# Optimization experiments

Measured on AMD Instinct MI355X. Metric: run time of the kernel, lower is better.

## Reference

```python
import jax, jax.numpy as jnp
import numpy as np

D = 1024
H = 16
HD = D // H
S = 2048
B = 2
INNER = 4 * D
EPS = 1e-5


def _layernorm(x, w, b):
    mu = jnp.mean(x, axis=-1, keepdims=True)
    var = jnp.mean(jnp.square(x - mu), axis=-1, keepdims=True)
    return (x - mu) * jax.lax.rsqrt(var + EPS) * w + b


def _rope(x, cos, sin):
    # x: [B, S, H, HD]; cos/sin: [S, HD//2]
    xe, xo = x[..., 0::2], x[..., 1::2]
    c = cos[None, :, None, :]
    s = sin[None, :, None, :]
    oe = xe * c - xo * s
    oo = xe * s + xo * c
    return jnp.stack([oe, oo], axis=-1).reshape(x.shape)


def setup_inputs() -> dict:
    key = jax.random.key(0)
    ks = jax.random.split(key, 12)
    hidden_states = jax.random.normal(ks[0], (B, S, D), dtype=jnp.float32)
    time_step_emb = jax.random.normal(ks[1], (B, 6 * D), dtype=jnp.float32)
    # causal additive mask [1,1,S,S]
    causal = jnp.tril(jnp.ones((S, S), dtype=bool))
    attention_mask = jnp.where(causal, 0.0, -1e9).astype(jnp.float32)[None, None]
    # proper RoPE tables
    inv_freq = 1.0 / (10000.0 ** (np.arange(0, HD, 2, dtype=np.float32) / HD))
    t = np.arange(S, dtype=np.float32)
    freqs = np.outer(t, inv_freq)  # [S, HD//2]
    rope_cos = jnp.asarray(np.cos(freqs))
    rope_sin = jnp.asarray(np.sin(freqs))
    p = 0.02
    params = dict(
        ln1_w=jnp.ones((D,), jnp.float32), ln1_b=jnp.zeros((D,), jnp.float32),
        ln2_w=jnp.ones((D,), jnp.float32), ln2_b=jnp.zeros((D,), jnp.float32),
        c_attn_w=jax.random.normal(ks[2], (D, 3 * D), jnp.float32) * p,
        c_attn_b=jnp.zeros((3 * D,), jnp.float32),
        c_proj_w=jax.random.normal(ks[3], (D, D), jnp.float32) * p,
        c_proj_b=jnp.zeros((D,), jnp.float32),
        fc_w=jax.random.normal(ks[4], (D, INNER), jnp.float32) * p,
        fc_b=jnp.zeros((INNER,), jnp.float32),
        proj_w=jax.random.normal(ks[5], (INNER, D), jnp.float32) * p,
        proj_b=jnp.zeros((D,), jnp.float32),
        scale_shift_table=jax.random.normal(ks[6], (6, D), jnp.float32) / np.sqrt(D),
    )
    return dict(hidden_states=hidden_states, attention_mask=attention_mask,
                time_step_emb=time_step_emb, rope_cos=rope_cos, rope_sin=rope_sin,
                **params)


def reference(hidden_states, attention_mask, time_step_emb, rope_cos, rope_sin,
              ln1_w, ln1_b, ln2_w, ln2_b, c_attn_w, c_attn_b, c_proj_w, c_proj_b,
              fc_w, fc_b, proj_w, proj_b, scale_shift_table):
    b = hidden_states.shape[0]
    mods = scale_shift_table[None] + time_step_emb.reshape(b, 6, D)  # [B,6,D]
    sh_msa, sc_msa, g_msa, sh_mlp, sc_mlp, g_mlp = [mods[:, i:i + 1] for i in range(6)]

    residual = hidden_states
    h = _layernorm(hidden_states, ln1_w, ln1_b) * (1.0 + sc_msa) + sh_msa

    qkv = h @ c_attn_w + c_attn_b  # [B,S,3D]
    q, k, v = jnp.split(qkv, 3, axis=-1)
    q = _rope(q.reshape(b, S, H, HD), rope_cos, rope_sin)
    k = _rope(k.reshape(b, S, H, HD), rope_cos, rope_sin)
    v = v.reshape(b, S, H, HD)
    scores = jnp.einsum('bqhd,bkhd->bhqk', q, k) / np.sqrt(float(HD))
    scores = scores + attention_mask
    attn = jax.nn.softmax(scores, axis=-1)
    out = jnp.einsum('bhqk,bkhd->bqhd', attn, v).reshape(b, S, D)
    attn_out = out @ c_proj_w + c_proj_b

    hidden = attn_out * g_msa + residual
    residual = hidden
    h = _layernorm(hidden, ln2_w, ln2_b) * (1.0 + sc_mlp) + sh_mlp
    h = jax.nn.gelu(h @ fc_w + fc_b, approximate=True)  # gelu_new (tanh approx)
    h = h @ proj_w + proj_b
    return h * g_mlp + residual
```

## Files before the change

### kernel.cpp

```cpp
#include <hip/hip_runtime.h>
#include <hip/hip_bf16.h>

#define D_MODEL 1024
#define N_HEADS 16
#define HEAD_DIM 64
#define SEQ 2048
#define BATCH 2
#define INNER_DIM 4096
#define ROWS (BATCH*SEQ)

using f32x4  = __attribute__((ext_vector_type(4))) float;
using bf16x8 = __attribute__((ext_vector_type(8))) short;

__device__ __forceinline__ void gl_lds16(const void* g, void* l) {
  __builtin_amdgcn_global_load_lds(
      (const __attribute__((address_space(1))) void*)g,
      (__attribute__((address_space(3))) void*)l, 16, 0, 0);
}

__device__ __forceinline__ float bf2f(unsigned short u) {
  union { unsigned int i; float f; } v; v.i = ((unsigned int)u) << 16; return v.f;
}
__device__ __forceinline__ unsigned short f2bf(float f) {
  union { float f; unsigned int i; } v; v.f = f;
  unsigned int x = v.i;
  return (unsigned short)((x + 0x7fffu + ((x >> 16) & 1u)) >> 16);
}

__device__ __forceinline__ float exp2fast(float x) {
  return __builtin_amdgcn_exp2f(x);
}

__device__ __forceinline__ float gelu_tanh(float x) {
  float x3 = x * x * x;
  float z = 0.7978845608028654f * (x + 0.044715f * x3);
  z = fminf(z, 15.0f);
  float e = __expf(2.0f * z);
  float th = (e - 1.0f) / (e + 1.0f);
  return 0.5f * x * (1.0f + th);
}

__global__ void transpose_convert(const float* __restrict__ in,
                                  unsigned short* __restrict__ out,
                                  int K, int N) {
  __shared__ float tile[32][33];
  int n0 = blockIdx.x * 32, k0 = blockIdx.y * 32;
  int tx = threadIdx.x, ty = threadIdx.y;
#pragma unroll
  for (int i = 0; i < 4; i++)
    tile[ty + i * 8][tx] = in[(size_t)(k0 + ty + i * 8) * N + n0 + tx];
  __syncthreads();
#pragma unroll
  for (int i = 0; i < 4; i++)
    out[(size_t)(n0 + ty + i * 8) * K + k0 + tx] = f2bf(tile[tx][ty + i * 8]);
}

template<int SH_IDX, int SC_IDX>
__global__ void ln_mod_kernel(const float* __restrict__ x,
                              const float* __restrict__ lw,
                              const float* __restrict__ lb,
                              const float* __restrict__ sst,
                              const float* __restrict__ temb,
                              unsigned short* __restrict__ out) {
  int row = blockIdx.x;
  int b = row >> 11;
  int t = threadIdx.x;
  const float* xr = x + (size_t)row * D_MODEL;
  float4 v = ((const float4*)xr)[t];
  float s = v.x + v.y + v.z + v.w;
  float s2 = v.x * v.x + v.y * v.y + v.z * v.z + v.w * v.w;
#pragma unroll
  for (int o = 1; o < 64; o <<= 1) { s += __shfl_xor(s, o); s2 += __shfl_xor(s2, o); }
  __shared__ float red[8];
  int wid = t >> 6, lane = t & 63;
  if (lane == 0) { red[wid] = s; red[4 + wid] = s2; }
  __syncthreads();
  s = red[0] + red[1] + red[2] + red[3];
  s2 = red[4] + red[5] + red[6] + red[7];
  float mu = s * (1.0f / D_MODEL);
  float var = s2 * (1.0f / D_MODEL) - mu * mu;
  float rs = rsqrtf(var + 1e-5f);
  int d0 = t * 4;
  float xv[4] = { v.x, v.y, v.z, v.w };
  ushort4 ov;
  unsigned short* po = (unsigned short*)&ov;
#pragma unroll
  for (int j = 0; j < 4; j++) {
    int d = d0 + j;
    float ln = (xv[j] - mu) * rs * lw[d] + lb[d];
    float sc = sst[SC_IDX * D_MODEL + d] + temb[b * 6 * D_MODEL + SC_IDX * D_MODEL + d];
    float sh = sst[SH_IDX * D_MODEL + d] + temb[b * 6 * D_MODEL + SH_IDX * D_MODEL + d];
    po[j] = f2bf(ln * (1.0f + sc) + sh);
  }
  *((ushort4*)(out + (size_t)row * D_MODEL + d0)) = ov;
}

enum { EPI_QKV = 0, EPI_RES = 1, EPI_GELU = 2, EPI_FINAL = 3 };

template<int EPI, int BMF>
__global__ __launch_bounds__(256, 2)
void gemm_kernel(const unsigned short* __restrict__ A,
                 const unsigned short* __restrict__ Bt,
                 const float* __restrict__ bias,
                 void* __restrict__ Cout,
                 int N, int K,
                 const float* __restrict__ sst,
                 const float* __restrict__ temb,
                 int g_idx,
                 const float* __restrict__ res,
                 const float* __restrict__ cosb,
                 const float* __restrict__ sinb) {
  constexpr int NBUF = 4;
  __shared__ unsigned short Alds[NBUF][BMF * 32 * 32];
  __shared__ unsigned short Blds[NBUF][128 * 32];
  const int t = threadIdx.x;
  const int w = t >> 6, l = t & 63;
  const int lg = l >> 4, ll = l & 15;
  const int wm = w >> 1, wn = w & 1;

  const int nx = gridDim.x;
  const int nwg = nx * gridDim.y;
  const int lid = blockIdx.y * nx + blockIdx.x;
  const int nid = (lid & 7) * (nwg >> 3) + (lid >> 3);
  const int m0 = (nid / nx) * (BMF * 32), n0 = (nid % nx) * 128;

  f32x4 acc[BMF][4] = {};

  auto stage = [&](int k0, int buf) {
#pragma unroll
    for (int i = 0; i < BMF / 2; i++) {
      int c = i * 256 + t;
      int row = c >> 2, ch = c & 3;
      int chs = ch ^ ((row >> 1) & 3);
      gl_lds16(A + (size_t)(m0 + row) * K + k0 + chs * 8, (char*)&Alds[buf][0] + c * 16);
    }
#pragma unroll
    for (int i = 0; i < 2; i++) {
      int c = i * 256 + t;
      int row = c >> 2, ch = c & 3;
      int chs = ch ^ ((row >> 1) & 3);
      gl_lds16(Bt + (size_t)(n0 + row) * K + k0 + chs * 8, (char*)&Blds[buf][0] + c * 16);
    }
  };

  auto comp = [&](int buf) {
    asm volatile("" ::: "memory");
    bf16x8 af[BMF], bfr[4];
#pragma unroll
    for (int mf = 0; mf < BMF; mf++) {
      int row = wm * (BMF * 16) + mf * 16 + ll;
      int ch = lg ^ ((row >> 1) & 3);
      af[mf] = *(const bf16x8*)((const char*)&Alds[buf][0] + row * 64 + ch * 16);
    }
#pragma unroll
    for (int nf = 0; nf < 4; nf++) {
      int row = wn * 64 + nf * 16 + ll;
      int ch = lg ^ ((row >> 1) & 3);
      bfr[nf] = *(const bf16x8*)((const char*)&Blds[buf][0] + row * 64 + ch * 16);
    }
#pragma unroll
    for (int mf = 0; mf < BMF; mf++)
#pragma unroll
      for (int nf = 0; nf < 4; nf++)
        acc[mf][nf] = __builtin_amdgcn_mfma_f32_16x16x32_bf16(af[mf], bfr[nf], acc[mf][nf], 0, 0, 0);
    asm volatile("" ::: "memory");
  };

  const int nk = K >> 5;
  stage(0, 0); stage(32, 1); stage(64, 2);
  int it = 0;
  for (; it + 3 < nk; ++it) {
    stage((it + 3) * 32, (it + 3) & 3);
    if constexpr (BMF == 4) asm volatile("s_waitcnt vmcnt(12)" ::: "memory");
    else                    asm volatile("s_waitcnt vmcnt(9)" ::: "memory");
    __builtin_amdgcn_s_barrier();
    comp(it & 3);
    __builtin_amdgcn_s_barrier();
  }
  if constexpr (BMF == 4) asm volatile("s_waitcnt vmcnt(8)" ::: "memory");
  else                    asm volatile("s_waitcnt vmcnt(6)" ::: "memory");
  __builtin_amdgcn_s_barrier(); comp(it & 3); __builtin_amdgcn_s_barrier(); ++it;
  if constexpr (BMF == 4) asm volatile("s_waitcnt vmcnt(4)" ::: "memory");
  else                    asm volatile("s_waitcnt vmcnt(3)" ::: "memory");
  __builtin_amdgcn_s_barrier(); comp(it & 3); __builtin_amdgcn_s_barrier(); ++it;
  asm volatile("s_waitcnt vmcnt(0)" ::: "memory");
  __builtin_amdgcn_s_barrier(); comp(it & 3); __builtin_amdgcn_s_barrier();

#pragma unroll
  for (int mf = 0; mf < BMF; mf++) {
#pragma unroll
    for (int nf = 0; nf < 4; nf++) {
      int col = n0 + wn * 64 + nf * 16 + ll;
      float bv = bias[col];
#pragma unroll
      for (int r = 0; r < 4; r++) {
        int row = m0 + wm * (BMF * 16) + mf * 16 + lg * 4 + r;
        float v = acc[mf][nf][r] + bv;
        if constexpr (EPI == EPI_QKV) {
          if (col < 2048) {
            float vp = __shfl_xor(v, 1);
            int sp = row & (SEQ - 1);
            int ip = (col & 63) >> 1;
            float cz = cosb[sp * 32 + ip], sz = sinb[sp * 32 + ip];
            float ov = (col & 1) ? (vp * sz + v * cz) : (v * cz - vp * sz);
            if (col < 1024) ov *= 0.18033688011112042f;
            v = ov;
          }
          ((unsigned short*)Cout)[(size_t)row * N + col] = f2bf(v);
        } else if constexpr (EPI == EPI_GELU) {
          ((unsigned short*)Cout)[(size_t)row * N + col] = f2bf(gelu_tanh(v));
        } else {
          int bb = row >> 11;
          float g = sst[g_idx * D_MODEL + col] + temb[bb * 6 * D_MODEL + g_idx * D_MODEL + col];
          ((float*)Cout)[(size_t)row * N + col] = v * g + res[(size_t)row * N + col];
        }
      }
    }
  }
}

__global__ __launch_bounds__(256, 4)
void attn_kernel(const unsigned short* __restrict__ qkv,
                 unsigned short* __restrict__ attn_o) {
  __shared__ unsigned short Klds[2][64 * 64];
  __shared__ unsigned short Vt[2][64 * 64];
  __shared__ unsigned short Plds[4][16 * 64];

  const int id = blockIdx.x;
  const int bh = id & 31;
  const int b = bh >> 4, h = bh & 15;
  const int q0 = (id >> 5) * 64;
  const int t = threadIdx.x;
  const int w = t >> 6, l = t & 63;
  const int lg = l >> 4, ll = l & 15;
  const int qw0 = q0 + w * 16;
  const int q_lane = qw0 + ll;

  bf16x8 qf[2];
  {
    const unsigned short* qb = qkv + (size_t)(b * SEQ + q_lane) * 3072 + h * 64;
    qf[0] = *(const bf16x8*)(qb + lg * 8);
    qf[1] = *(const bf16x8*)(qb + 32 + lg * 8);
  }

  const int kp = t & 31, dg = t >> 5;

  f32x4 oacc[4] = {};
  float mrun = -1e30f, lrun = 0.0f;

  {
#pragma unroll
    for (int i = 0; i < 2; i++) {
      int c = i * 256 + t;
      int kr = c >> 3, cc = c & 7;
      gl_lds16(qkv + (size_t)(b * SEQ + kr) * 3072 + 1024 + h * 64 + (cc ^ (kr & 7)) * 8,
               (char*)&Klds[0][0] + c * 16);
    }
    const unsigned short* vp = qkv + (size_t)(b * SEQ + 2 * kp) * 3072 + 2048 + h * 64 + dg * 8;
    union { uint4 u; unsigned short s[8]; } a0, a1;
    a0.u = *(const uint4*)vp;
    a1.u = *(const uint4*)(vp + 3072);
    unsigned int* vt32 = (unsigned int*)&Vt[0][0];
#pragma unroll
    for (int i = 0; i < 8; i++)
      vt32[(dg * 8 + i) * 32 + (((kp >> 2) ^ i) << 2) + (kp & 3)] =
          (unsigned int)a0.s[i] | ((unsigned int)a1.s[i] << 16);
  }
  __syncthreads();

  int buf = 0;
  for (int k0 = 0; k0 <= q0; k0 += 64) {
    const bool has_next = (k0 + 64 <= q0);
    union { uint4 u; unsigned short s[8]; } n0, n1;
    if (has_next) {
#pragma unroll
      for (int i = 0; i < 2; i++) {
        int c = i * 256 + t;
        int kr = c >> 3, cc = c & 7;
        gl_lds16(qkv + (size_t)(b * SEQ + k0 + 64 + kr) * 3072 + 1024 + h * 64 + (cc ^ (kr & 7)) * 8,
                 (char*)&Klds[buf ^ 1][0] + c * 16);
      }
      const unsigned short* vp =
          qkv + (size_t)(b * SEQ + k0 + 64 + 2 * kp) * 3072 + 2048 + h * 64 + dg * 8;
      n0.u = *(const uint4*)vp;
      n1.u = *(const uint4*)(vp + 3072);
    }

    f32x4 s[4] = {};
#pragma unroll
    for (int kk = 0; kk < 2; kk++) {
#pragma unroll
      for (int nf = 0; nf < 4; nf++) {
        int key = nf * 16 + ll;
        int cc = (kk * 4 + lg) ^ (key & 7);
        bf16x8 kf = *(const bf16x8*)((const char*)&Klds[buf][0] + key * 128 + cc * 16);
        s[nf] = __builtin_amdgcn_mfma_f32_16x16x32_bf16(kf, qf[kk], s[nf], 0, 0, 0);
      }
    }
    if (k0 == q0) {
#pragma unroll
      for (int nf = 0; nf < 4; nf++) {
        int key = k0 + nf * 16 + lg * 4;
#pragma unroll
        for (int r = 0; r < 4; r++)
          if (key + r > q_lane) s[nf][r] = -1e30f;
      }
    }
    float mx = -1e30f;
#pragma unroll
    for (int nf = 0; nf < 4; nf++)
#pragma unroll
      for (int r = 0; r < 4; r++) mx = fmaxf(mx, s[nf][r]);
    mx = fmaxf(mx, __shfl_xor(mx, 16));
    mx = fmaxf(mx, __shfl_xor(mx, 32));
    float mnew = fmaxf(mrun, mx);
    float alpha = exp2fast(mrun - mnew);
    mrun = mnew;
    float ps = 0.0f;
#pragma unroll
    for (int nf = 0; nf < 4; nf++)
#pragma unroll
      for (int r = 0; r < 4; r++) {
        float p = exp2fast(s[nf][r] - mnew);
        s[nf][r] = p;
        ps += p;
      }
    ps += __shfl_xor(ps, 16);
    ps += __shfl_xor(ps, 32);
    lrun = lrun * alpha + ps;
#pragma unroll
    for (int nf = 0; nf < 4; nf++)
#pragma unroll
      for (int r = 0; r < 4; r++) oacc[nf][r] *= alpha;

#pragma unroll
    for (int nf = 0; nf < 4; nf++) {
      unsigned int lo = (unsigned int)f2bf(s[nf][0]) | ((unsigned int)f2bf(s[nf][1]) << 16);
      unsigned int hi = (unsigned int)f2bf(s[nf][2]) | ((unsigned int)f2bf(s[nf][3]) << 16);
      int chunk = (nf * 2 + (lg >> 1)) ^ (ll & 7);
      uint2 pv; pv.x = lo; pv.y = hi;
      *(uint2*)((char*)&Plds[w][0] + ll * 128 + chunk * 16 + (lg & 1) * 8) = pv;
    }
    bf16x8 pb[2];
#pragma unroll
    for (int kk = 0; kk < 2; kk++) {
      int pc = (kk * 4 + lg) ^ (ll & 7);
      pb[kk] = *(const bf16x8*)((char*)&Plds[w][0] + ll * 128 + pc * 16);
    }
#pragma unroll
    for (int nf = 0; nf < 4; nf++) {
      int d = nf * 16 + ll;
#pragma unroll
      for (int kk = 0; kk < 2; kk++) {
        int vc = (kk * 4 + lg) ^ (d & 7);
        bf16x8 vb = *(const bf16x8*)((const char*)&Vt[buf][0] + d * 128 + vc * 16);
        oacc[nf] = __builtin_amdgcn_mfma_f32_16x16x32_bf16(vb, pb[kk], oacc[nf], 0, 0, 0);
      }
    }
    if (has_next) {
      unsigned int* vt32 = (unsigned int*)&Vt[buf ^ 1][0];
#pragma unroll
      for (int i = 0; i < 8; i++)
        vt32[(dg * 8 + i) * 32 + (((kp >> 2) ^ i) << 2) + (kp & 3)] =
            (unsigned int)n0.s[i] | ((unsigned int)n1.s[i] << 16);
    }
    __syncthreads();
    buf ^= 1;
  }

  float rl = 1.0f / lrun;
#pragma unroll
  for (int nf = 0; nf < 4; nf++) {
    ushort4 ov;
    ov.x = f2bf(oacc[nf][0] * rl);
    ov.y = f2bf(oacc[nf][1] * rl);
    ov.z = f2bf(oacc[nf][2] * rl);
    ov.w = f2bf(oacc[nf][3] * rl);
    *(ushort4*)(attn_o + (size_t)(b * SEQ + q_lane) * D_MODEL + h * 64 + nf * 16 + lg * 4) = ov;
  }
}

extern "C" void kernel_launch(void* const* d_in, const int* in_sizes, int n_in,
                              void* d_out, int out_size, void* d_ws, size_t ws_size,
                              hipStream_t stream) {
  const float* hidden_states = (const float*)d_in[0];
  const float* temb     = (const float*)d_in[2];
  const float* rope_cos = (const float*)d_in[3];
  const float* rope_sin = (const float*)d_in[4];
  const float* ln1_w    = (const float*)d_in[5];
  const float* ln1_b    = (const float*)d_in[6];
  const float* ln2_w    = (const float*)d_in[7];
  const float* ln2_b    = (const float*)d_in[8];
  const float* c_attn_w = (const float*)d_in[9];
  const float* c_attn_b = (const float*)d_in[10];
  const float* c_proj_w = (const float*)d_in[11];
  const float* c_proj_b = (const float*)d_in[12];
  const float* fc_w     = (const float*)d_in[13];
  const float* fc_b     = (const float*)d_in[14];
  const float* proj_w   = (const float*)d_in[15];
  const float* proj_b   = (const float*)d_in[16];
  const float* sst      = (const float*)d_in[17];

  char* ws = (char*)d_ws;
  unsigned short* wqkv  = (unsigned short*)(ws + 0);
  unsigned short* wproj = (unsigned short*)(ws + 6291456);
  unsigned short* wfc   = (unsigned short*)(ws + 8388608);
  unsigned short* wp2   = (unsigned short*)(ws + 16777216);
  unsigned short* hln   = (unsigned short*)(ws + 25165824);
  unsigned short* qkvb  = (unsigned short*)(ws + 33554432);
  unsigned short* attno = (unsigned short*)(ws + 58720256);
  unsigned short* h3    = (unsigned short*)(ws + 33554432);
  float*          hidden = (float*)(ws + 67108864);

  dim3 tb(32, 8);
  transpose_convert<<<dim3(3072 / 32, 1024 / 32), tb, 0, stream>>>(c_attn_w, wqkv, 1024, 3072);
  transpose_convert<<<dim3(1024 / 32, 1024 / 32), tb, 0, stream>>>(c_proj_w, wproj, 1024, 1024);
  transpose_convert<<<dim3(4096 / 32, 1024 / 32), tb, 0, stream>>>(fc_w, wfc, 1024, 4096);
  transpose_convert<<<dim3(1024 / 32, 4096 / 32), tb, 0, stream>>>(proj_w, wp2, 4096, 1024);

  ln_mod_kernel<0, 1><<<ROWS, 256, 0, stream>>>(hidden_states, ln1_w, ln1_b, sst, temb, hln);

  gemm_kernel<EPI_QKV, 4><<<dim3(3072 / 128, ROWS / 128), 256, 0, stream>>>(
      hln, wqkv, c_attn_b, qkvb, 3072, 1024, nullptr, nullptr, 0, nullptr, rope_cos, rope_sin);

  attn_kernel<<<dim3(32 * 32), 256, 0, stream>>>(qkvb, attno);

  gemm_kernel<EPI_RES, 2><<<dim3(1024 / 128, ROWS / 64), 256, 0, stream>>>(
      attno, wproj, c_proj_b, hidden, 1024, 1024, sst, temb, 2, hidden_states, nullptr, nullptr);

  ln_mod_kernel<3, 4><<<ROWS, 256, 0, stream>>>(hidden, ln2_w, ln2_b, sst, temb, hln);

  gemm_kernel<EPI_GELU, 4><<<dim3(4096 / 128, ROWS / 128), 256, 0, stream>>>(
      hln, wfc, fc_b, h3, 4096, 1024, nullptr, nullptr, 0, nullptr, nullptr, nullptr);

  gemm_kernel<EPI_FINAL, 2><<<dim3(1024 / 128, ROWS / 64), 256, 0, stream>>>(
      h3, wp2, proj_b, d_out, 1024, 4096, sst, temb, 5, hidden, nullptr, nullptr);
}
```

Baseline: 301.6 us.

## Split-K the narrow GEMMs, double-buffer GEMM pipeline, reverse attention tile order

The two N=1024 GEMMs (attention projection and MLP down-projection) now use split-K over two z-slices. Each slice writes bf16 partials, and a new elementwise kernel sums them and applies bias, gate and residual. The GEMM pipeline drops from four LDS buffers to two, launch bounds rise to four blocks per SM, and all GEMMs use 64-row tiles, so more workgroups are resident. Attention now launches the heavier causal query tiles first to balance the tail. The costs are extra partial-sum traffic, two extra launches, bf16 rounding of the partials, and shallower prefetch.

```diff
diff --git a/kernel.cpp b/kernel.cpp
--- a/kernel.cpp
+++ b/kernel.cpp
@@ -95,28 +95,24 @@
   *((ushort4*)(out + (size_t)row * D_MODEL + d0)) = ov;
 }
 
-enum { EPI_QKV = 0, EPI_RES = 1, EPI_GELU = 2, EPI_FINAL = 3 };
+enum { EPI_QKV = 0, EPI_GELU = 2, EPI_PART = 3 };
 
 template<int EPI, int BMF>
-__global__ __launch_bounds__(256, 2)
+__global__ __launch_bounds__(256, 4)
 void gemm_kernel(const unsigned short* __restrict__ A,
                  const unsigned short* __restrict__ Bt,
                  const float* __restrict__ bias,
-                 void* __restrict__ Cout,
-                 int N, int K,
-                 const float* __restrict__ sst,
-                 const float* __restrict__ temb,
-                 int g_idx,
-                 const float* __restrict__ res,
+                 void* C0, void* C1,
+                 int N, int Ksub, int Kstride,
                  const float* __restrict__ cosb,
                  const float* __restrict__ sinb) {
-  constexpr int NBUF = 4;
-  __shared__ unsigned short Alds[NBUF][BMF * 32 * 32];
-  __shared__ unsigned short Blds[NBUF][128 * 32];
+  __shared__ unsigned short Alds[2][BMF * 32 * 32];
+  __shared__ unsigned short Blds[2][128 * 32];
   const int t = threadIdx.x;
   const int w = t >> 6, l = t & 63;
   const int lg = l >> 4, ll = l & 15;
   const int wm = w >> 1, wn = w & 1;
+  const int kbase = blockIdx.z * Ksub;
 
   const int nx = gridDim.x;
   const int nwg = nx * gridDim.y;
@@ -124,27 +120,42 @@
   const int nid = (lid & 7) * (nwg >> 3) + (lid >> 3);
   const int m0 = (nid / nx) * (BMF * 32), n0 = (nid % nx) * 128;
 
+  void* Cout = blockIdx.z ? C1 : C0;
+
   f32x4 acc[BMF][4] = {};
 
   auto stage = [&](int k0, int buf) {
 #pragma unroll
-    for (int i = 0; i < BMF / 2; i++) {
-      int c = i * 256 + t;
+    for (int c = t; c < BMF * 128; c += 256) {
       int row = c >> 2, ch = c & 3;
       int chs = ch ^ ((row >> 1) & 3);
-      gl_lds16(A + (size_t)(m0 + row) * K + k0 + chs * 8, (char*)&Alds[buf][0] + c * 16);
+      gl_lds16(A + (size_t)(m0 + row) * Kstride + kbase + k0 + chs * 8,
+               (char*)&Alds[buf][0] + c * 16);
     }
 #pragma unroll
     for (int i = 0; i < 2; i++) {
       int c = i * 256 + t;
       int row = c >> 2, ch = c & 3;
       int chs = ch ^ ((row >> 1) & 3);
-      gl_lds16(Bt + (size_t)(n0 + row) * K + k0 + chs * 8, (char*)&Blds[buf][0] + c * 16);
+      gl_lds16(Bt + (size_t)(n0 + row) * Kstride + kbase + k0 + chs * 8,
+               (char*)&Blds[buf][0] + c * 16);
     }
   };
 
-  auto comp = [&](int buf) {
+  stage(0, 0);
+  int buf = 0;
+  const int nk = Ksub >> 5;
+  for (int it = 0; it < nk; ++it) {
+    if (it + 1 < nk) {
+      stage((it + 1) * 32, buf ^ 1);
+      if constexpr (BMF == 4) asm volatile("s_waitcnt vmcnt(4)" ::: "memory");
+      else                    asm volatile("s_waitcnt vmcnt(3)" ::: "memory");
+    } else {
+      asm volatile("s_waitcnt vmcnt(0)" ::: "memory");
+    }
+    __builtin_amdgcn_s_barrier();
     asm volatile("" ::: "memory");
+
     bf16x8 af[BMF], bfr[4];
 #pragma unroll
     for (int mf = 0; mf < BMF; mf++) {
@@ -163,35 +174,18 @@
 #pragma unroll
       for (int nf = 0; nf < 4; nf++)
         acc[mf][nf] = __builtin_amdgcn_mfma_f32_16x16x32_bf16(af[mf], bfr[nf], acc[mf][nf], 0, 0, 0);
+
     asm volatile("" ::: "memory");
-  };
-
-  const int nk = K >> 5;
-  stage(0, 0); stage(32, 1); stage(64, 2);
-  int it = 0;
-  for (; it + 3 < nk; ++it) {
-    stage((it + 3) * 32, (it + 3) & 3);
-    if constexpr (BMF == 4) asm volatile("s_waitcnt vmcnt(12)" ::: "memory");
-    else                    asm volatile("s_waitcnt vmcnt(9)" ::: "memory");
     __builtin_amdgcn_s_barrier();
-    comp(it & 3);
-    __builtin_amdgcn_s_barrier();
-  }
-  if constexpr (BMF == 4) asm volatile("s_waitcnt vmcnt(8)" ::: "memory");
-  else                    asm volatile("s_waitcnt vmcnt(6)" ::: "memory");
-  __builtin_amdgcn_s_barrier(); comp(it & 3); __builtin_amdgcn_s_barrier(); ++it;
-  if constexpr (BMF == 4) asm volatile("s_waitcnt vmcnt(4)" ::: "memory");
-  else                    asm volatile("s_waitcnt vmcnt(3)" ::: "memory");
-  __builtin_amdgcn_s_barrier(); comp(it & 3); __builtin_amdgcn_s_barrier(); ++it;
-  asm volatile("s_waitcnt vmcnt(0)" ::: "memory");
-  __builtin_amdgcn_s_barrier(); comp(it & 3); __builtin_amdgcn_s_barrier();
+    buf ^= 1;
+  }
 
 #pragma unroll
   for (int mf = 0; mf < BMF; mf++) {
 #pragma unroll
     for (int nf = 0; nf < 4; nf++) {
       int col = n0 + wn * 64 + nf * 16 + ll;
-      float bv = bias[col];
+      float bv = (EPI == EPI_PART) ? 0.0f : bias[col];
 #pragma unroll
       for (int r = 0; r < 4; r++) {
         int row = m0 + wm * (BMF * 16) + mf * 16 + lg * 4 + r;
@@ -210,13 +204,40 @@
         } else if constexpr (EPI == EPI_GELU) {
           ((unsigned short*)Cout)[(size_t)row * N + col] = f2bf(gelu_tanh(v));
         } else {
-          int bb = row >> 11;
-          float g = sst[g_idx * D_MODEL + col] + temb[bb * 6 * D_MODEL + g_idx * D_MODEL + col];
-          ((float*)Cout)[(size_t)row * N + col] = v * g + res[(size_t)row * N + col];
+          ((unsigned short*)Cout)[(size_t)row * N + col] = f2bf(v);
         }
       }
     }
   }
+}
+
+__global__ void reduce_gated(const unsigned short* __restrict__ p0,
+                             const unsigned short* __restrict__ p1,
+                             const float* __restrict__ bias,
+                             const float* __restrict__ sst,
+                             const float* __restrict__ temb,
+                             int g_idx,
+                             const float* __restrict__ resid,
+                             float* __restrict__ out) {
+  int i = blockIdx.x * 256 + threadIdx.x;
+  int idx = i * 4;
+  int col = idx & 1023;
+  int b = idx >> 21;
+  ushort4 a0 = *(const ushort4*)(p0 + idx);
+  ushort4 a1 = *(const ushort4*)(p1 + idx);
+  float4 rv = *(const float4*)(resid + idx);
+  float4 o;
+  const unsigned short* s0 = (const unsigned short*)&a0;
+  const unsigned short* s1 = (const unsigned short*)&a1;
+  float* po = (float*)&o;
+  const float* pr = (const float*)&rv;
+#pragma unroll
+  for (int j = 0; j < 4; j++) {
+    float s = bf2f(s0[j]) + bf2f(s1[j]) + bias[col + j];
+    float g = sst[g_idx * D_MODEL + col + j] + temb[b * 6 * D_MODEL + g_idx * D_MODEL + col + j];
+    po[j] = s * g + pr[j];
+  }
+  *(float4*)(out + idx) = o;
 }
 
 __global__ __launch_bounds__(256, 4)
@@ -229,7 +250,7 @@
   const int id = blockIdx.x;
   const int bh = id & 31;
   const int b = bh >> 4, h = bh & 15;
-  const int q0 = (id >> 5) * 64;
+  const int q0 = (31 - (id >> 5)) * 64;
   const int t = threadIdx.x;
   const int w = t >> 6, l = t & 63;
   const int lg = l >> 4, ll = l & 15;
@@ -409,8 +430,12 @@
   unsigned short* hln   = (unsigned short*)(ws + 25165824);
   unsigned short* qkvb  = (unsigned short*)(ws + 33554432);
   unsigned short* attno = (unsigned short*)(ws + 58720256);
-  unsigned short* h3    = (unsigned short*)(ws + 33554432);
   float*          hidden = (float*)(ws + 67108864);
+  unsigned short* rp0 = (unsigned short*)(ws + 33554432);
+  unsigned short* rp1 = (unsigned short*)(ws + 41943040);
+  unsigned short* h3  = (unsigned short*)(ws + 33554432);
+  unsigned short* fp0 = (unsigned short*)(ws + 0);
+  unsigned short* fp1 = (unsigned short*)(ws + 8388608);
 
   dim3 tb(32, 8);
   transpose_convert<<<dim3(3072 / 32, 1024 / 32), tb, 0, stream>>>(c_attn_w, wqkv, 1024, 3072);
@@ -420,19 +445,23 @@
 
   ln_mod_kernel<0, 1><<<ROWS, 256, 0, stream>>>(hidden_states, ln1_w, ln1_b, sst, temb, hln);
 
-  gemm_kernel<EPI_QKV, 4><<<dim3(3072 / 128, ROWS / 128), 256, 0, stream>>>(
-      hln, wqkv, c_attn_b, qkvb, 3072, 1024, nullptr, nullptr, 0, nullptr, rope_cos, rope_sin);
+  gemm_kernel<EPI_QKV, 2><<<dim3(3072 / 128, ROWS / 64, 1), 256, 0, stream>>>(
+      hln, wqkv, c_attn_b, qkvb, qkvb, 3072, 1024, 1024, rope_cos, rope_sin);
 
   attn_kernel<<<dim3(32 * 32), 256, 0, stream>>>(qkvb, attno);
 
-  gemm_kernel<EPI_RES, 2><<<dim3(1024 / 128, ROWS / 64), 256, 0, stream>>>(
-      attno, wproj, c_proj_b, hidden, 1024, 1024, sst, temb, 2, hidden_states, nullptr, nullptr);
+  gemm_kernel<EPI_PART, 2><<<dim3(1024 / 128, ROWS / 64, 2), 256, 0, stream>>>(
+      attno, wproj, c_proj_b, rp0, rp1, 1024, 512, 1024, nullptr, nullptr);
+  reduce_gated<<<(ROWS * D_MODEL / 4) / 256, 256, 0, stream>>>(
+      rp0, rp1, c_proj_b, sst, temb, 2, hidden_states, hidden);
 
   ln_mod_kernel<3, 4><<<ROWS, 256, 0, stream>>>(hidden, ln2_w, ln2_b, sst, temb, hln);
 
-  gemm_kernel<EPI_GELU, 4><<<dim3(4096 / 128, ROWS / 128), 256, 0, stream>>>(
-      hln, wfc, fc_b, h3, 4096, 1024, nullptr, nullptr, 0, nullptr, nullptr, nullptr);
-
-  gemm_kernel<EPI_FINAL, 2><<<dim3(1024 / 128, ROWS / 64), 256, 0, stream>>>(
-      h3, wp2, proj_b, d_out, 1024, 4096, sst, temb, 5, hidden, nullptr, nullptr);
-}
+  gemm_kernel<EPI_GELU, 2><<<dim3(4096 / 128, ROWS / 64, 1), 256, 0, stream>>>(
+      hln, wfc, fc_b, h3, h3, 4096, 1024, 1024, nullptr, nullptr);
+
+  gemm_kernel<EPI_PART, 2><<<dim3(1024 / 128, ROWS / 64, 2), 256, 0, stream>>>(
+      h3, wp2, proj_b, fp0, fp1, 1024, 2048, 4096, nullptr, nullptr);
+  reduce_gated<<<(ROWS * D_MODEL / 4) / 256, 256, 0, stream>>>(
+      fp0, fp1, proj_b, sst, temb, 5, hidden, (float*)d_out);
+}
```

Result: faster. 293.5 us (-2.7%).
